# Kernel optimization log

Measured on AMD Instinct MI355X. Metric: run time of the kernel, lower is better.

Reference implementation:

```python
import jax, jax.numpy as jnp
import numpy as np

B, S, D = 4, 2048, 2048
E = 8            # num_experts
TOP_K = 2
H = 1408         # intermediate_size per expert
SH = 2 * H       # shared expert intermediate (shared_experts=2)


def setup_inputs() -> dict:
    key = jax.random.key(0)
    ks = jax.random.split(key, 8)
    sc = 0.02
    return {
        "hidden_states": jax.random.normal(ks[0], (B, S, D), jnp.float32),
        "gate_w": jax.random.normal(ks[1], (E, D), jnp.float32) * sc,   # torch Linear weight [out,in]
        "w1": jax.random.normal(ks[2], (E, H, D), jnp.float32) * sc,    # gate_proj per expert
        "w3": jax.random.normal(ks[3], (E, H, D), jnp.float32) * sc,    # up_proj per expert
        "w2": jax.random.normal(ks[4], (E, D, H), jnp.float32) * sc,    # down_proj per expert
        "sw1": jax.random.normal(ks[5], (SH, D), jnp.float32) * sc,
        "sw3": jax.random.normal(ks[6], (SH, D), jnp.float32) * sc,
        "sw2": jax.random.normal(ks[7], (D, SH), jnp.float32) * sc,
    }


def reference(hidden_states, gate_w, w1, w3, w2, sw1, sw3, sw2):
    b, s, d = hidden_states.shape
    x = hidden_states.reshape(-1, d)                      # [T, D]
    logits = x @ gate_w.T                                 # [T, E]
    rw, sel = jax.lax.top_k(logits, TOP_K)                # [T, K]
    rw = jax.nn.softmax(rw, axis=-1)                      # norm_topk_prob=True
    onehot = jax.nn.one_hot(sel, E, dtype=x.dtype)        # [T, K, E]
    token_mask = onehot.sum(axis=1)                       # [T, E] in {0,1}
    # NOTE: faithful to the source quirk: expert_weights.sum(dim=-1) on a flat
    # masked gather sums routing weights over ALL tokens selecting the expert,
    # producing one scalar per expert.
    s_e = (rw[..., None] * onehot).sum(axis=(0, 1))       # [E]
    combine = token_mask * s_e                            # [T, E]
    # per-expert SwiGLU MLP on all tokens (dense combine form of gather/scatter)
    g = jnp.einsum('td,ehd->eth', x, w1)                  # [E, T, H]
    u = jnp.einsum('td,ehd->eth', x, w3)
    a = jax.nn.silu(g) * u
    y = jnp.einsum('eth,edh->etd', a, w2)                 # [E, T, D]
    out = jnp.einsum('te,etd->td', combine, y)            # [T, D]
    shared = (jax.nn.silu(x @ sw1.T) * (x @ sw3.T)) @ sw2.T
    out = out + shared
    return out.reshape(b, s, d)
```

## Files before the change

kernel.cpp:

```cpp
#include <hip/hip_runtime.h>
#include <hip/hip_bf16.h>
#include <stdint.h>

#define T_TOK 8192
#define DIM   2048
#define NEXP  8
#define HDIM  1408
#define SHDIM 2816

typedef __attribute__((ext_vector_type(8))) short bfrag;
typedef __attribute__((ext_vector_type(4))) float f32x4;

__device__ __forceinline__ short f2bf(float f) {
    union { float f; uint32_t u; } v; v.f = f;
    return (short)((v.u + 0x8000u) >> 16);
}

__device__ __forceinline__ bfrag cvt8(float4 a, float4 b) {
    bfrag r;
    r[0] = f2bf(a.x); r[1] = f2bf(a.y); r[2] = f2bf(a.z); r[3] = f2bf(a.w);
    r[4] = f2bf(b.x); r[5] = f2bf(b.y); r[6] = f2bf(b.z); r[7] = f2bf(b.w);
    return r;
}

__device__ __forceinline__ void gload16(const void* g, void* l) {
    __builtin_amdgcn_global_load_lds(
        (__attribute__((address_space(1))) void*)(g),
        (__attribute__((address_space(3))) void*)(l), 16, 0, 0);
}

#define MFMA16(a, b, c) __builtin_amdgcn_mfma_f32_16x16x32_bf16((a), (b), (c), 0, 0, 0)


__global__ __launch_bounds__(256) void gate_kernel(
    const float* __restrict__ x, const float* __restrict__ gw,
    int* __restrict__ sel, int* __restrict__ meta, float* __restrict__ s_e)
{
    __shared__ float g[NEXP * DIM];
    for (int i = threadIdx.x; i < NEXP * DIM; i += 256) g[i] = gw[i];
    __syncthreads();
    const int wid = threadIdx.x >> 6, lane = threadIdx.x & 63;
    for (int it = 0; it < 8; ++it) {
        const int t = blockIdx.x * 32 + wid * 8 + it;
        float acc[NEXP];
#pragma unroll
        for (int e = 0; e < NEXP; ++e) acc[e] = 0.f;
        const float4* xr = (const float4*)(x + (size_t)t * DIM);
        for (int j = 0; j < DIM / 4; j += 64) {
            float4 xv = xr[j + lane];
#pragma unroll
            for (int e = 0; e < NEXP; ++e) {
                float4 gv = *(const float4*)&g[e * DIM + (j + lane) * 4];
                acc[e] += xv.x * gv.x + xv.y * gv.y + xv.z * gv.z + xv.w * gv.w;
            }
        }
#pragma unroll
        for (int e = 0; e < NEXP; ++e)
            for (int o = 32; o; o >>= 1) acc[e] += __shfl_xor(acc[e], o);
        if (lane == 0) {
            int e0 = 0; float v0 = acc[0];
#pragma unroll
            for (int e = 1; e < NEXP; ++e) if (acc[e] > v0) { v0 = acc[e]; e0 = e; }
            int e1 = -1; float v1 = -3.4e38f;
#pragma unroll
            for (int e = 0; e < NEXP; ++e) if (e != e0 && acc[e] > v1) { v1 = acc[e]; e1 = e; }
            float p0 = 1.f / (1.f + __expf(v1 - v0));
            float p1 = 1.f - p0;
            sel[2 * t] = e0; sel[2 * t + 1] = e1;
            atomicAdd(&s_e[e0], p0); atomicAdd(&s_e[e1], p1);
            atomicAdd(&meta[e0], 1); atomicAdd(&meta[e1], 1);
        }
    }
}

__global__ void scan_kernel(int* meta) {
    if (threadIdx.x == 0) {
        int acc = 0;
        for (int e = 0; e < NEXP; ++e) {
            meta[16 + e] = acc;
            meta[8 + e]  = acc;
            acc += meta[e];
        }
        meta[24] = acc;
    }
}

__global__ __launch_bounds__(256) void fill_kernel(
    const int* __restrict__ sel, int* __restrict__ meta, int* __restrict__ list)
{
    const int t = blockIdx.x * 256 + threadIdx.x;
    int e0 = sel[2 * t], e1 = sel[2 * t + 1];
    int p0 = atomicAdd(&meta[8 + e0], 1); list[p0] = t;
    int p1 = atomicAdd(&meta[8 + e1], 1); list[p1] = t;
}

__global__ __launch_bounds__(256) void cvt_kernel(
    const float* __restrict__ in, __hip_bfloat16* __restrict__ out, int n8)
{
    int i = blockIdx.x * 256 + threadIdx.x;
    const int stride = gridDim.x * 256;
    for (; i < n8; i += stride) {
        const float4* p = (const float4*)(in + (size_t)i * 8);
        float4 a = p[0], b = p[1];
        *(bfrag*)(out + (size_t)i * 8) = cvt8(a, b);
    }
}


template<int N, bool GATHER>
__global__ __launch_bounds__(512, 2) void up_v3(
    const __hip_bfloat16* __restrict__ X,
    const __hip_bfloat16* __restrict__ W1,
    const __hip_bfloat16* __restrict__ W3,
    __hip_bfloat16* __restrict__ act,
    const int* __restrict__ list,
    const int* __restrict__ meta)
{
    constexpr int K = DIM;
    constexpr int NT = K / 64;
    constexpr int nx = N / 128, ny = T_TOK / 256, nz = GATHER ? NEXP : 1;
    constexpr int nwg = nx * ny * nz, cpx = nwg / 8;
    const int bid = (int)blockIdx.x + nx * ((int)blockIdx.y + ny * (int)blockIdx.z);
    const int virt = (bid & 7) * cpx + (bid >> 3);
    const int xi = virt % nx;
    const int rest = virt / nx;
    const int yi = rest % ny;
    const int e = rest / ny;

    int count, base;
    if (GATHER) {
        count = meta[e]; base = meta[16 + e];
        if (yi * 256 >= count) return;
    } else { count = T_TOK; base = 0; }
    const int m0 = yi * 256, n0 = xi * 128;

    __shared__ alignas(16) short As[2][256 * 64];
    __shared__ alignas(16) short B1s[2][128 * 64];
    __shared__ alignas(16) short B3s[2][128 * 64];

    const int tid = threadIdx.x, wid = tid >> 6, lane = tid & 63;
    const int rlo = lane >> 3;
    const int swslot = (lane & 7) ^ rlo;

    const __hip_bfloat16* pA[4];
#pragma unroll
    for (int q = 0; q < 4; ++q) {
        int row = (q * 8 + wid) * 8 + rlo;
        int r = m0 + row; if (r > count - 1) r = count - 1;
        int ga = GATHER ? list[base + r] : r;
        pA[q] = X + (size_t)ga * K + swslot * 8;
    }
    const __hip_bfloat16* pB1[2];
    const __hip_bfloat16* pB3[2];
#pragma unroll
    for (int q = 0; q < 2; ++q) {
        int row = (q * 8 + wid) * 8 + rlo;
        pB1[q] = W1 + ((size_t)e * N + n0 + row) * K + swslot * 8;
        pB3[q] = W3 + ((size_t)e * N + n0 + row) * K + swslot * 8;
    }

#define STAGE_UP(T, BUF) do { const int k0_ = (T) * 64;                         \
    _Pragma("unroll") for (int q = 0; q < 4; ++q)                               \
        gload16(pA[q] + k0_, &As[BUF][(q * 8 + wid) * 512]);                    \
    _Pragma("unroll") for (int q = 0; q < 2; ++q) {                             \
        gload16(pB1[q] + k0_, &B1s[BUF][(q * 8 + wid) * 512]);                  \
        gload16(pB3[q] + k0_, &B3s[BUF][(q * 8 + wid) * 512]); } } while (0)

    const int wm = wid >> 2, wn = wid & 3;
    const int l15 = lane & 15, lhi = lane >> 4;

    f32x4 accg[8][2], accu[8][2];
#pragma unroll
    for (int i = 0; i < 8; ++i)
#pragma unroll
        for (int j = 0; j < 2; ++j) { accg[i][j] = 0.f; accu[i][j] = 0.f; }

    STAGE_UP(0, 0);
    __syncthreads();
    int cur = 0;
#pragma unroll 1
    for (int t = 0; t < NT; ++t) {
        if (t + 1 < NT) STAGE_UP(t + 1, cur ^ 1);
        __builtin_amdgcn_sched_barrier(0);
        bfrag b1f[2][2], b3f[2][2];
#pragma unroll
        for (int j = 0; j < 2; ++j)
#pragma unroll
            for (int kk = 0; kk < 2; ++kk) {
                int rb = wn * 32 + j * 16 + l15;
                int c = kk * 4 + lhi;
                int off = rb * 128 + ((c ^ (rb & 7)) << 4);
                b1f[j][kk] = *(const bfrag*)((const char*)B1s[cur] + off);
                b3f[j][kk] = *(const bfrag*)((const char*)B3s[cur] + off);
            }
        __builtin_amdgcn_s_setprio(1);
#pragma unroll
        for (int i = 0; i < 8; ++i) {
            int ra = wm * 128 + i * 16 + l15;
            const char* abase = (const char*)As[cur] + ra * 128;
            bfrag a0 = *(const bfrag*)(abase + ((lhi       ^ (ra & 7)) << 4));
            bfrag a1 = *(const bfrag*)(abase + (((4 + lhi) ^ (ra & 7)) << 4));
#pragma unroll
            for (int j = 0; j < 2; ++j) {
                accg[i][j] = MFMA16(a0, b1f[j][0], accg[i][j]);
                accu[i][j] = MFMA16(a0, b3f[j][0], accu[i][j]);
                accg[i][j] = MFMA16(a1, b1f[j][1], accg[i][j]);
                accu[i][j] = MFMA16(a1, b3f[j][1], accu[i][j]);
            }
        }
        __builtin_amdgcn_s_setprio(0);
        __syncthreads();
        cur ^= 1;
    }
#undef STAGE_UP

#pragma unroll
    for (int i = 0; i < 8; ++i)
#pragma unroll
        for (int r = 0; r < 4; ++r) {
            int m = wm * 128 + i * 16 + lhi * 4 + r;
            if (m0 + m < count) {
#pragma unroll
                for (int j = 0; j < 2; ++j) {
                    float gg = accg[i][j][r];
                    float uu = accu[i][j][r];
                    float a = gg / (1.f + __expf(-gg)) * uu;
                    int n = n0 + wn * 32 + j * 16 + l15;
                    act[(size_t)(base + m0 + m) * N + n] = __float2bfloat16(a);
                }
            }
        }
}

template<int KD, bool SCATTER>
__global__ __launch_bounds__(512, 2) void down_v3(
    const __hip_bfloat16* __restrict__ A,
    const __hip_bfloat16* __restrict__ W2,
    float* __restrict__ out,
    const int* __restrict__ list,
    const int* __restrict__ meta,
    const float* __restrict__ s_e)
{
    constexpr int N = DIM;
    constexpr int NT = KD / 64;
    constexpr int nx = N / 256, ny = T_TOK / 256, nz = SCATTER ? NEXP : 1;
    constexpr int nwg = nx * ny * nz, cpx = nwg / 8;
    const int bid = (int)blockIdx.x + nx * ((int)blockIdx.y + ny * (int)blockIdx.z);
    const int virt = (bid & 7) * cpx + (bid >> 3);
    const int xi = virt % nx;
    const int rest = virt / nx;
    const int yi = rest % ny;
    const int e = rest / ny;

    int count, base;
    if (SCATTER) {
        count = meta[e]; base = meta[16 + e];
        if (yi * 256 >= count) return;
    } else { count = T_TOK; base = 0; }
    const int m0 = yi * 256, n0 = xi * 256;

    __shared__ alignas(16) short As[2][256 * 64];
    __shared__ alignas(16) short Bs[2][256 * 64];
    __shared__ int tok_s[256];

    const int tid = threadIdx.x, wid = tid >> 6, lane = tid & 63;
    if (SCATTER && tid < 256) {
        int r = m0 + tid; if (r > count - 1) r = count - 1;
        tok_s[tid] = list[base + r];
    }
    const int rlo = lane >> 3;
    const int swslot = (lane & 7) ^ rlo;

    const __hip_bfloat16* pA[4];
    const __hip_bfloat16* pB[4];
#pragma unroll
    for (int q = 0; q < 4; ++q) {
        int row = (q * 8 + wid) * 8 + rlo;
        int r = m0 + row; if (r > count - 1) r = count - 1;
        pA[q] = A  + (size_t)(base + r) * KD + swslot * 8;
        pB[q] = W2 + ((size_t)e * N + n0 + row) * KD + swslot * 8;
    }

#define STAGE_DN(T, BUF) do { const int k0_ = (T) * 64;                         \
    _Pragma("unroll") for (int q = 0; q < 4; ++q) {                             \
        gload16(pA[q] + k0_, &As[BUF][(q * 8 + wid) * 512]);                    \
        gload16(pB[q] + k0_, &Bs[BUF][(q * 8 + wid) * 512]); } } while (0)

    const int wm = wid >> 2, wn = wid & 3;
    const int l15 = lane & 15, lhi = lane >> 4;

    f32x4 acc[8][4];
#pragma unroll
    for (int i = 0; i < 8; ++i)
#pragma unroll
        for (int j = 0; j < 4; ++j) acc[i][j] = 0.f;

    STAGE_DN(0, 0);
    __syncthreads();
    int cur = 0;
#pragma unroll 1
    for (int t = 0; t < NT; ++t) {
        if (t + 1 < NT) STAGE_DN(t + 1, cur ^ 1);
        __builtin_amdgcn_sched_barrier(0);
        bfrag bf[4][2];
#pragma unroll
        for (int j = 0; j < 4; ++j)
#pragma unroll
            for (int kk = 0; kk < 2; ++kk) {
                int rb = wn * 64 + j * 16 + l15;
                int c = kk * 4 + lhi;
                bf[j][kk] = *(const bfrag*)((const char*)Bs[cur] + rb * 128 + ((c ^ (rb & 7)) << 4));
            }
        __builtin_amdgcn_s_setprio(1);
#pragma unroll
        for (int i = 0; i < 8; ++i) {
            int ra = wm * 128 + i * 16 + l15;
            const char* abase = (const char*)As[cur] + ra * 128;
            bfrag a0 = *(const bfrag*)(abase + ((lhi       ^ (ra & 7)) << 4));
            bfrag a1 = *(const bfrag*)(abase + (((4 + lhi) ^ (ra & 7)) << 4));
#pragma unroll
            for (int j = 0; j < 4; ++j) {
                acc[i][j] = MFMA16(a0, bf[j][0], acc[i][j]);
                acc[i][j] = MFMA16(a1, bf[j][1], acc[i][j]);
            }
        }
        __builtin_amdgcn_s_setprio(0);
        __syncthreads();
        cur ^= 1;
    }
#undef STAGE_DN

    const float scale = SCATTER ? s_e[e] : 1.0f;
#pragma unroll
    for (int i = 0; i < 8; ++i)
#pragma unroll
        for (int r = 0; r < 4; ++r) {
            int m = wm * 128 + i * 16 + lhi * 4 + r;
            if (m0 + m < count) {
#pragma unroll
                for (int j = 0; j < 4; ++j) {
                    int n = n0 + wn * 64 + j * 16 + l15;
                    float v = acc[i][j][r] * scale;
                    if (SCATTER) atomicAdd(&out[(size_t)tok_s[m] * DIM + n], v);
                    else         out[(size_t)(m0 + m) * DIM + n] = v;
                }
            }
        }
}

extern "C" void kernel_launch(void* const* d_in, const int* in_sizes, int n_in,
                              void* d_out, int out_size, void* d_ws, size_t ws_size,
                              hipStream_t stream) {
    const float* x   = (const float*)d_in[0];
    const float* gw  = (const float*)d_in[1];
    const float* w1  = (const float*)d_in[2];
    const float* w3  = (const float*)d_in[3];
    const float* w2  = (const float*)d_in[4];
    const float* sw1 = (const float*)d_in[5];
    const float* sw3 = (const float*)d_in[6];
    const float* sw2 = (const float*)d_in[7];
    float* out = (float*)d_out;

    const size_t SZ_X   = (size_t)T_TOK * DIM * 2;
    const size_t SZ_W   = (size_t)NEXP * HDIM * DIM * 2;
    const size_t SZ_SW  = (size_t)SHDIM * DIM * 2;
    const size_t SZ_ACT = (size_t)2 * T_TOK * HDIM * 2;
    const size_t need = SZ_X + 3 * SZ_W + 3 * SZ_SW + SZ_ACT
                      + (size_t)4 * T_TOK * sizeof(int) + 512;
    if (need > ws_size) return;

    char* p = (char*)d_ws;
    __hip_bfloat16* xbf   = (__hip_bfloat16*)p; p += SZ_X;
    __hip_bfloat16* w1bf  = (__hip_bfloat16*)p; p += SZ_W;
    __hip_bfloat16* w3bf  = (__hip_bfloat16*)p; p += SZ_W;
    __hip_bfloat16* w2bf  = (__hip_bfloat16*)p; p += SZ_W;
    __hip_bfloat16* sw1bf = (__hip_bfloat16*)p; p += SZ_SW;
    __hip_bfloat16* sw3bf = (__hip_bfloat16*)p; p += SZ_SW;
    __hip_bfloat16* sw2bf = (__hip_bfloat16*)p; p += SZ_SW;
    __hip_bfloat16* act   = (__hip_bfloat16*)p; p += SZ_ACT;
    int* list = (int*)p; p += (size_t)2 * T_TOK * sizeof(int);
    int* sel  = (int*)p; p += (size_t)2 * T_TOK * sizeof(int);
    int* meta = (int*)p;
    float* s_e = (float*)(meta + 32);

    hipMemsetAsync(meta, 0, 256, stream);
    gate_kernel<<<T_TOK / 32, 256, 0, stream>>>(x, gw, sel, meta, s_e);
    scan_kernel<<<1, 64, 0, stream>>>(meta);
    fill_kernel<<<T_TOK / 256, 256, 0, stream>>>(sel, meta, list);

    cvt_kernel<<<2048, 256, 0, stream>>>(x,   xbf,   T_TOK * DIM / 8);
    cvt_kernel<<<2048, 256, 0, stream>>>(w1,  w1bf,  NEXP * HDIM * DIM / 8);
    cvt_kernel<<<2048, 256, 0, stream>>>(w3,  w3bf,  NEXP * HDIM * DIM / 8);
    cvt_kernel<<<2048, 256, 0, stream>>>(w2,  w2bf,  NEXP * HDIM * DIM / 8);
    cvt_kernel<<<2048, 256, 0, stream>>>(sw1, sw1bf, SHDIM * DIM / 8);
    cvt_kernel<<<2048, 256, 0, stream>>>(sw3, sw3bf, SHDIM * DIM / 8);
    cvt_kernel<<<2048, 256, 0, stream>>>(sw2, sw2bf, SHDIM * DIM / 8);

    up_v3<SHDIM, false><<<dim3(SHDIM / 128, T_TOK / 256, 1), 512, 0, stream>>>(
        xbf, sw1bf, sw3bf, act, nullptr, meta);
    down_v3<SHDIM, false><<<dim3(DIM / 256, T_TOK / 256, 1), 512, 0, stream>>>(
        act, sw2bf, out, nullptr, meta, s_e);
    up_v3<HDIM, true><<<dim3(HDIM / 128, T_TOK / 256, NEXP), 512, 0, stream>>>(
        xbf, w1bf, w3bf, act, list, meta);
    down_v3<HDIM, true><<<dim3(DIM / 256, T_TOK / 256, NEXP), 512, 0, stream>>>(
        act, w2bf, out, list, meta, s_e);
}
```

Measured before the change: 1.181 ms.

## Split K-tiles into half stages, fuse conversions, replace atomic scatter with combine pass

The GEMM main loops now split each 64-wide K tile into two 32-wide sub-stages. Each sub-stage is prefetched one step ahead and guarded by explicit vmcnt waits and barriers instead of full __syncthreads, with a new 4-slot LDS swizzle. The x-to-bf16 conversion moves into the gate kernel, and the six weight conversions are fused into one launch. The routed down-projection writes bf16 per-slot outputs to a scratch buffer that aliases the start of the workspace, and a new combine kernel adds the weighted results per token, replacing float atomics. This aims to remove atomic contention, launch overhead and pipeline stalls. It adds bf16 rounding of expert outputs and a workspace aliasing risk, since yscr overlaps xbf and the converted weights.

```diff
diff --git a/kernel.cpp b/kernel.cpp
--- a/kernel.cpp
+++ b/kernel.cpp
@@ -10,10 +10,15 @@
 
 typedef __attribute__((ext_vector_type(8))) short bfrag;
 typedef __attribute__((ext_vector_type(4))) float f32x4;
+typedef __attribute__((ext_vector_type(4))) short s16x4;
 
 __device__ __forceinline__ short f2bf(float f) {
     union { float f; uint32_t u; } v; v.f = f;
     return (short)((v.u + 0x8000u) >> 16);
+}
+__device__ __forceinline__ float bf2f(short s) {
+    union { uint32_t u; float f; } v; v.u = ((uint32_t)(uint16_t)s) << 16;
+    return v.f;
 }
 
 __device__ __forceinline__ bfrag cvt8(float4 a, float4 b) {
@@ -30,10 +35,12 @@
 }
 
 #define MFMA16(a, b, c) __builtin_amdgcn_mfma_f32_16x16x32_bf16((a), (b), (c), 0, 0, 0)
+#define SWZ4(r) (((r) & 3) ^ (((r) >> 2) & 3))
 
 
 __global__ __launch_bounds__(256) void gate_kernel(
     const float* __restrict__ x, const float* __restrict__ gw,
+    __hip_bfloat16* __restrict__ xbf,
     int* __restrict__ sel, int* __restrict__ meta, float* __restrict__ s_e)
 {
     __shared__ float g[NEXP * DIM];
@@ -48,6 +55,8 @@
         const float4* xr = (const float4*)(x + (size_t)t * DIM);
         for (int j = 0; j < DIM / 4; j += 64) {
             float4 xv = xr[j + lane];
+            s16x4 xv16 = { f2bf(xv.x), f2bf(xv.y), f2bf(xv.z), f2bf(xv.w) };
+            *(s16x4*)&xbf[(size_t)t * DIM + (j + lane) * 4] = xv16;
 #pragma unroll
             for (int e = 0; e < NEXP; ++e) {
                 float4 gv = *(const float4*)&g[e * DIM + (j + lane) * 4];
@@ -86,29 +95,46 @@
 }
 
 __global__ __launch_bounds__(256) void fill_kernel(
-    const int* __restrict__ sel, int* __restrict__ meta, int* __restrict__ list)
+    const int* __restrict__ sel, int* __restrict__ meta,
+    int* __restrict__ list, int2* __restrict__ slots)
 {
     const int t = blockIdx.x * 256 + threadIdx.x;
     int e0 = sel[2 * t], e1 = sel[2 * t + 1];
     int p0 = atomicAdd(&meta[8 + e0], 1); list[p0] = t;
     int p1 = atomicAdd(&meta[8 + e1], 1); list[p1] = t;
-}
-
-__global__ __launch_bounds__(256) void cvt_kernel(
-    const float* __restrict__ in, __hip_bfloat16* __restrict__ out, int n8)
-{
-    int i = blockIdx.x * 256 + threadIdx.x;
+    slots[t] = make_int2(p0, p1);
+}
+
+#define C1 2883584
+#define C2 5767168
+#define C3 8650752
+#define C4 9371648
+#define C5 10092544
+#define C6 10813440
+__global__ __launch_bounds__(256) void cvt6_kernel(
+    const float* __restrict__ s0, const float* __restrict__ s1, const float* __restrict__ s2,
+    const float* __restrict__ s3, const float* __restrict__ s4, const float* __restrict__ s5,
+    __hip_bfloat16* __restrict__ d0, __hip_bfloat16* __restrict__ d1, __hip_bfloat16* __restrict__ d2,
+    __hip_bfloat16* __restrict__ d3, __hip_bfloat16* __restrict__ d4, __hip_bfloat16* __restrict__ d5)
+{
     const int stride = gridDim.x * 256;
-    for (; i < n8; i += stride) {
-        const float4* p = (const float4*)(in + (size_t)i * 8);
+    for (int i = blockIdx.x * 256 + threadIdx.x; i < C6; i += stride) {
+        const float* s; __hip_bfloat16* d; int off;
+        if      (i < C1) { s = s0; d = d0; off = i; }
+        else if (i < C2) { s = s1; d = d1; off = i - C1; }
+        else if (i < C3) { s = s2; d = d2; off = i - C2; }
+        else if (i < C4) { s = s3; d = d3; off = i - C3; }
+        else if (i < C5) { s = s4; d = d4; off = i - C4; }
+        else             { s = s5; d = d5; off = i - C5; }
+        const float4* p = (const float4*)(s + (size_t)off * 8);
         float4 a = p[0], b = p[1];
-        *(bfrag*)(out + (size_t)i * 8) = cvt8(a, b);
+        *(bfrag*)(d + (size_t)off * 8) = cvt8(a, b);
     }
 }
 
 
 template<int N, bool GATHER>
-__global__ __launch_bounds__(512, 2) void up_v3(
+__global__ __launch_bounds__(512, 2) void up_v4(
     const __hip_bfloat16* __restrict__ X,
     const __hip_bfloat16* __restrict__ W1,
     const __hip_bfloat16* __restrict__ W3,
@@ -134,40 +160,33 @@
     } else { count = T_TOK; base = 0; }
     const int m0 = yi * 256, n0 = xi * 128;
 
-    __shared__ alignas(16) short As[2][256 * 64];
-    __shared__ alignas(16) short B1s[2][128 * 64];
-    __shared__ alignas(16) short B3s[2][128 * 64];
+    __shared__ alignas(16) short As[2][2][256 * 32];
+    __shared__ alignas(16) short B1s[2][2][128 * 32];
+    __shared__ alignas(16) short B3s[2][2][128 * 32];
 
     const int tid = threadIdx.x, wid = tid >> 6, lane = tid & 63;
-    const int rlo = lane >> 3;
-    const int swslot = (lane & 7) ^ rlo;
-
-    const __hip_bfloat16* pA[4];
-#pragma unroll
-    for (int q = 0; q < 4; ++q) {
-        int row = (q * 8 + wid) * 8 + rlo;
-        int r = m0 + row; if (r > count - 1) r = count - 1;
+    const int srow = tid >> 2, dslot = tid & 3;
+    const int sswz = dslot ^ SWZ4(srow);
+
+    const __hip_bfloat16* pA[2];
+#pragma unroll
+    for (int q = 0; q < 2; ++q) {
+        int r = m0 + q * 128 + srow; if (r > count - 1) r = count - 1;
         int ga = GATHER ? list[base + r] : r;
-        pA[q] = X + (size_t)ga * K + swslot * 8;
-    }
-    const __hip_bfloat16* pB1[2];
-    const __hip_bfloat16* pB3[2];
-#pragma unroll
-    for (int q = 0; q < 2; ++q) {
-        int row = (q * 8 + wid) * 8 + rlo;
-        pB1[q] = W1 + ((size_t)e * N + n0 + row) * K + swslot * 8;
-        pB3[q] = W3 + ((size_t)e * N + n0 + row) * K + swslot * 8;
-    }
-
-#define STAGE_UP(T, BUF) do { const int k0_ = (T) * 64;                         \
-    _Pragma("unroll") for (int q = 0; q < 4; ++q)                               \
-        gload16(pA[q] + k0_, &As[BUF][(q * 8 + wid) * 512]);                    \
-    _Pragma("unroll") for (int q = 0; q < 2; ++q) {                             \
-        gload16(pB1[q] + k0_, &B1s[BUF][(q * 8 + wid) * 512]);                  \
-        gload16(pB3[q] + k0_, &B3s[BUF][(q * 8 + wid) * 512]); } } while (0)
+        pA[q] = X + (size_t)ga * K + sswz * 8;
+    }
+    const __hip_bfloat16* pB1 = W1 + ((size_t)e * N + n0 + srow) * K + sswz * 8;
+    const __hip_bfloat16* pB3 = W3 + ((size_t)e * N + n0 + srow) * K + sswz * 8;
+
+#define STAGE_UP(K0, KK, BUF) do {                                              \
+    gload16(pA[0] + (K0) + (KK) * 32, &As[BUF][KK][tid * 8]);                   \
+    gload16(pA[1] + (K0) + (KK) * 32, &As[BUF][KK][4096 + tid * 8]);            \
+    gload16(pB1   + (K0) + (KK) * 32, &B1s[BUF][KK][tid * 8]);                  \
+    gload16(pB3   + (K0) + (KK) * 32, &B3s[BUF][KK][tid * 8]); } while (0)
 
     const int wm = wid >> 2, wn = wid & 3;
     const int l15 = lane & 15, lhi = lane >> 4;
+    const int lswz = (lhi ^ SWZ4(l15)) * 8;
 
     f32x4 accg[8][2], accu[8][2];
 #pragma unroll
@@ -175,44 +194,46 @@
 #pragma unroll
         for (int j = 0; j < 2; ++j) { accg[i][j] = 0.f; accu[i][j] = 0.f; }
 
-    STAGE_UP(0, 0);
-    __syncthreads();
-    int cur = 0;
+    STAGE_UP(0, 0, 0);
+    STAGE_UP(0, 1, 0);
+    asm volatile("s_waitcnt vmcnt(4)" ::: "memory");
+    __builtin_amdgcn_s_barrier();
+    __builtin_amdgcn_sched_barrier(0);
+
 #pragma unroll 1
     for (int t = 0; t < NT; ++t) {
-        if (t + 1 < NT) STAGE_UP(t + 1, cur ^ 1);
-        __builtin_amdgcn_sched_barrier(0);
-        bfrag b1f[2][2], b3f[2][2];
-#pragma unroll
-        for (int j = 0; j < 2; ++j)
-#pragma unroll
-            for (int kk = 0; kk < 2; ++kk) {
+        const int cur = t & 1;
+        const int tpk0 = (t + 1 < NT ? t + 1 : NT - 1) * 64;
+#pragma unroll
+        for (int kk = 0; kk < 2; ++kk) {
+            bfrag b1f[2], b3f[2];
+#pragma unroll
+            for (int j = 0; j < 2; ++j) {
                 int rb = wn * 32 + j * 16 + l15;
-                int c = kk * 4 + lhi;
-                int off = rb * 128 + ((c ^ (rb & 7)) << 4);
-                b1f[j][kk] = *(const bfrag*)((const char*)B1s[cur] + off);
-                b3f[j][kk] = *(const bfrag*)((const char*)B3s[cur] + off);
-            }
-        __builtin_amdgcn_s_setprio(1);
-#pragma unroll
-        for (int i = 0; i < 8; ++i) {
-            int ra = wm * 128 + i * 16 + l15;
-            const char* abase = (const char*)As[cur] + ra * 128;
-            bfrag a0 = *(const bfrag*)(abase + ((lhi       ^ (ra & 7)) << 4));
-            bfrag a1 = *(const bfrag*)(abase + (((4 + lhi) ^ (ra & 7)) << 4));
-#pragma unroll
-            for (int j = 0; j < 2; ++j) {
-                accg[i][j] = MFMA16(a0, b1f[j][0], accg[i][j]);
-                accu[i][j] = MFMA16(a0, b3f[j][0], accu[i][j]);
-                accg[i][j] = MFMA16(a1, b1f[j][1], accg[i][j]);
-                accu[i][j] = MFMA16(a1, b3f[j][1], accu[i][j]);
-            }
-        }
-        __builtin_amdgcn_s_setprio(0);
-        __syncthreads();
-        cur ^= 1;
+                b1f[j] = *(const bfrag*)&B1s[cur][kk][rb * 32 + lswz];
+                b3f[j] = *(const bfrag*)&B3s[cur][kk][rb * 32 + lswz];
+            }
+            STAGE_UP(tpk0, kk, cur ^ 1);
+            __builtin_amdgcn_s_barrier();
+            __builtin_amdgcn_s_setprio(1);
+#pragma unroll
+            for (int i = 0; i < 8; ++i) {
+                int ra = wm * 128 + i * 16 + l15;
+                bfrag a = *(const bfrag*)&As[cur][kk][ra * 32 + lswz];
+#pragma unroll
+                for (int j = 0; j < 2; ++j) {
+                    accg[i][j] = MFMA16(a, b1f[j], accg[i][j]);
+                    accu[i][j] = MFMA16(a, b3f[j], accu[i][j]);
+                }
+            }
+            __builtin_amdgcn_s_setprio(0);
+            asm volatile("s_waitcnt vmcnt(4)" ::: "memory");
+            __builtin_amdgcn_s_barrier();
+            __builtin_amdgcn_sched_barrier(0);
+        }
     }
 #undef STAGE_UP
+    asm volatile("s_waitcnt vmcnt(0)" ::: "memory");
 
 #pragma unroll
     for (int i = 0; i < 8; ++i)
@@ -232,18 +253,17 @@
         }
 }
 
-template<int KD, bool SCATTER>
-__global__ __launch_bounds__(512, 2) void down_v3(
+template<int KD, bool TO_BF16>
+__global__ __launch_bounds__(512, 2) void down_v4(
     const __hip_bfloat16* __restrict__ A,
     const __hip_bfloat16* __restrict__ W2,
     float* __restrict__ out,
-    const int* __restrict__ list,
-    const int* __restrict__ meta,
-    const float* __restrict__ s_e)
+    __hip_bfloat16* __restrict__ yscr,
+    const int* __restrict__ meta)
 {
     constexpr int N = DIM;
     constexpr int NT = KD / 64;
-    constexpr int nx = N / 256, ny = T_TOK / 256, nz = SCATTER ? NEXP : 1;
+    constexpr int nx = N / 256, ny = T_TOK / 256, nz = TO_BF16 ? NEXP : 1;
     constexpr int nwg = nx * ny * nz, cpx = nwg / 8;
     const int bid = (int)blockIdx.x + nx * ((int)blockIdx.y + ny * (int)blockIdx.z);
     const int virt = (bid & 7) * cpx + (bid >> 3);
@@ -253,41 +273,37 @@
     const int e = rest / ny;
 
     int count, base;
-    if (SCATTER) {
+    if (TO_BF16) {
         count = meta[e]; base = meta[16 + e];
         if (yi * 256 >= count) return;
     } else { count = T_TOK; base = 0; }
     const int m0 = yi * 256, n0 = xi * 256;
 
-    __shared__ alignas(16) short As[2][256 * 64];
-    __shared__ alignas(16) short Bs[2][256 * 64];
-    __shared__ int tok_s[256];
+    __shared__ alignas(16) short As[2][2][256 * 32];
+    __shared__ alignas(16) short Bs[2][2][256 * 32];
 
     const int tid = threadIdx.x, wid = tid >> 6, lane = tid & 63;
-    if (SCATTER && tid < 256) {
-        int r = m0 + tid; if (r > count - 1) r = count - 1;
-        tok_s[tid] = list[base + r];
-    }
-    const int rlo = lane >> 3;
-    const int swslot = (lane & 7) ^ rlo;
-
-    const __hip_bfloat16* pA[4];
-    const __hip_bfloat16* pB[4];
-#pragma unroll
-    for (int q = 0; q < 4; ++q) {
-        int row = (q * 8 + wid) * 8 + rlo;
-        int r = m0 + row; if (r > count - 1) r = count - 1;
-        pA[q] = A  + (size_t)(base + r) * KD + swslot * 8;
-        pB[q] = W2 + ((size_t)e * N + n0 + row) * KD + swslot * 8;
-    }
-
-#define STAGE_DN(T, BUF) do { const int k0_ = (T) * 64;                         \
-    _Pragma("unroll") for (int q = 0; q < 4; ++q) {                             \
-        gload16(pA[q] + k0_, &As[BUF][(q * 8 + wid) * 512]);                    \
-        gload16(pB[q] + k0_, &Bs[BUF][(q * 8 + wid) * 512]); } } while (0)
+    const int srow = tid >> 2, dslot = tid & 3;
+    const int sswz = dslot ^ SWZ4(srow);
+
+    const __hip_bfloat16* pA[2];
+    const __hip_bfloat16* pB[2];
+#pragma unroll
+    for (int q = 0; q < 2; ++q) {
+        int r = m0 + q * 128 + srow; if (r > count - 1) r = count - 1;
+        pA[q] = A  + (size_t)(base + r) * KD + sswz * 8;
+        pB[q] = W2 + ((size_t)e * N + n0 + q * 128 + srow) * KD + sswz * 8;
+    }
+
+#define STAGE_DN(K0, KK, BUF) do {                                              \
+    gload16(pA[0] + (K0) + (KK) * 32, &As[BUF][KK][tid * 8]);                   \
+    gload16(pA[1] + (K0) + (KK) * 32, &As[BUF][KK][4096 + tid * 8]);            \
+    gload16(pB[0] + (K0) + (KK) * 32, &Bs[BUF][KK][tid * 8]);                   \
+    gload16(pB[1] + (K0) + (KK) * 32, &Bs[BUF][KK][4096 + tid * 8]); } while (0)
 
     const int wm = wid >> 2, wn = wid & 3;
     const int l15 = lane & 15, lhi = lane >> 4;
+    const int lswz = (lhi ^ SWZ4(l15)) * 8;
 
     f32x4 acc[8][4];
 #pragma unroll
@@ -295,42 +311,44 @@
 #pragma unroll
         for (int j = 0; j < 4; ++j) acc[i][j] = 0.f;
 
-    STAGE_DN(0, 0);
-    __syncthreads();
-    int cur = 0;
+    STAGE_DN(0, 0, 0);
+    STAGE_DN(0, 1, 0);
+    asm volatile("s_waitcnt vmcnt(4)" ::: "memory");
+    __builtin_amdgcn_s_barrier();
+    __builtin_amdgcn_sched_barrier(0);
+
 #pragma unroll 1
     for (int t = 0; t < NT; ++t) {
-        if (t + 1 < NT) STAGE_DN(t + 1, cur ^ 1);
-        __builtin_amdgcn_sched_barrier(0);
-        bfrag bf[4][2];
-#pragma unroll
-        for (int j = 0; j < 4; ++j)
-#pragma unroll
-            for (int kk = 0; kk < 2; ++kk) {
+        const int cur = t & 1;
+        const int tpk0 = (t + 1 < NT ? t + 1 : NT - 1) * 64;
+#pragma unroll
+        for (int kk = 0; kk < 2; ++kk) {
+            bfrag bf[4];
+#pragma unroll
+            for (int j = 0; j < 4; ++j) {
                 int rb = wn * 64 + j * 16 + l15;
-                int c = kk * 4 + lhi;
-                bf[j][kk] = *(const bfrag*)((const char*)Bs[cur] + rb * 128 + ((c ^ (rb & 7)) << 4));
-            }
-        __builtin_amdgcn_s_setprio(1);
-#pragma unroll
-        for (int i = 0; i < 8; ++i) {
-            int ra = wm * 128 + i * 16 + l15;
-            const char* abase = (const char*)As[cur] + ra * 128;
-            bfrag a0 = *(const bfrag*)(abase + ((lhi       ^ (ra & 7)) << 4));
-            bfrag a1 = *(const bfrag*)(abase + (((4 + lhi) ^ (ra & 7)) << 4));
-#pragma unroll
-            for (int j = 0; j < 4; ++j) {
-                acc[i][j] = MFMA16(a0, bf[j][0], acc[i][j]);
-                acc[i][j] = MFMA16(a1, bf[j][1], acc[i][j]);
-            }
-        }
-        __builtin_amdgcn_s_setprio(0);
-        __syncthreads();
-        cur ^= 1;
+                bf[j] = *(const bfrag*)&Bs[cur][kk][rb * 32 + lswz];
+            }
+            STAGE_DN(tpk0, kk, cur ^ 1);
+            __builtin_amdgcn_s_barrier();
+            __builtin_amdgcn_s_setprio(1);
+#pragma unroll
+            for (int i = 0; i < 8; ++i) {
+                int ra = wm * 128 + i * 16 + l15;
+                bfrag a = *(const bfrag*)&As[cur][kk][ra * 32 + lswz];
+#pragma unroll
+                for (int j = 0; j < 4; ++j)
+                    acc[i][j] = MFMA16(a, bf[j], acc[i][j]);
+            }
+            __builtin_amdgcn_s_setprio(0);
+            asm volatile("s_waitcnt vmcnt(4)" ::: "memory");
+            __builtin_amdgcn_s_barrier();
+            __builtin_amdgcn_sched_barrier(0);
+        }
     }
 #undef STAGE_DN
-
-    const float scale = SCATTER ? s_e[e] : 1.0f;
+    asm volatile("s_waitcnt vmcnt(0)" ::: "memory");
+
 #pragma unroll
     for (int i = 0; i < 8; ++i)
 #pragma unroll
@@ -340,12 +358,38 @@
 #pragma unroll
                 for (int j = 0; j < 4; ++j) {
                     int n = n0 + wn * 64 + j * 16 + l15;
-                    float v = acc[i][j][r] * scale;
-                    if (SCATTER) atomicAdd(&out[(size_t)tok_s[m] * DIM + n], v);
-                    else         out[(size_t)(m0 + m) * DIM + n] = v;
+                    if (TO_BF16)
+                        yscr[(size_t)(base + m0 + m) * DIM + n] = __float2bfloat16(acc[i][j][r]);
+                    else
+                        out[(size_t)(m0 + m) * DIM + n] = acc[i][j][r];
                 }
             }
         }
+}
+
+__global__ __launch_bounds__(256) void combine_kernel(
+    float* __restrict__ out, const __hip_bfloat16* __restrict__ yscr,
+    const int* __restrict__ sel, const int2* __restrict__ slots,
+    const float* __restrict__ s_e)
+{
+    const int t = blockIdx.x;
+    const int d = threadIdx.x * 8;
+    const int2 sl = slots[t];
+    const float se0 = s_e[sel[2 * t]];
+    const float se1 = s_e[sel[2 * t + 1]];
+    bfrag y0 = *(const bfrag*)&yscr[(size_t)sl.x * DIM + d];
+    bfrag y1 = *(const bfrag*)&yscr[(size_t)sl.y * DIM + d];
+    float4* o = (float4*)(out + (size_t)t * DIM + d);
+    float4 o0 = o[0], o1 = o[1];
+    o0.x += se0 * bf2f(y0[0]) + se1 * bf2f(y1[0]);
+    o0.y += se0 * bf2f(y0[1]) + se1 * bf2f(y1[1]);
+    o0.z += se0 * bf2f(y0[2]) + se1 * bf2f(y1[2]);
+    o0.w += se0 * bf2f(y0[3]) + se1 * bf2f(y1[3]);
+    o1.x += se0 * bf2f(y0[4]) + se1 * bf2f(y1[4]);
+    o1.y += se0 * bf2f(y0[5]) + se1 * bf2f(y1[5]);
+    o1.z += se0 * bf2f(y0[6]) + se1 * bf2f(y1[6]);
+    o1.w += se0 * bf2f(y0[7]) + se1 * bf2f(y1[7]);
+    o[0] = o0; o[1] = o1;
 }
 
 extern "C" void kernel_launch(void* const* d_in, const int* in_sizes, int n_in,
@@ -366,7 +410,8 @@
     const size_t SZ_SW  = (size_t)SHDIM * DIM * 2;
     const size_t SZ_ACT = (size_t)2 * T_TOK * HDIM * 2;
     const size_t need = SZ_X + 3 * SZ_W + 3 * SZ_SW + SZ_ACT
-                      + (size_t)4 * T_TOK * sizeof(int) + 512;
+                      + (size_t)4 * T_TOK * sizeof(int)
+                      + (size_t)2 * T_TOK * sizeof(int)  + 512;
     if (need > ws_size) return;
 
     char* p = (char*)d_ws;
@@ -378,30 +423,28 @@
     __hip_bfloat16* sw3bf = (__hip_bfloat16*)p; p += SZ_SW;
     __hip_bfloat16* sw2bf = (__hip_bfloat16*)p; p += SZ_SW;
     __hip_bfloat16* act   = (__hip_bfloat16*)p; p += SZ_ACT;
-    int* list = (int*)p; p += (size_t)2 * T_TOK * sizeof(int);
-    int* sel  = (int*)p; p += (size_t)2 * T_TOK * sizeof(int);
-    int* meta = (int*)p;
-    float* s_e = (float*)(meta + 32);
+    int*  list  = (int*)p;  p += (size_t)2 * T_TOK * sizeof(int);
+    int*  sel   = (int*)p;  p += (size_t)2 * T_TOK * sizeof(int);
+    int2* slots = (int2*)p; p += (size_t)2 * T_TOK * sizeof(int);
+    int*  meta  = (int*)p;
+    float* s_e  = (float*)(meta + 32);
+    __hip_bfloat16* yscr = (__hip_bfloat16*)d_ws;
 
     hipMemsetAsync(meta, 0, 256, stream);
-    gate_kernel<<<T_TOK / 32, 256, 0, stream>>>(x, gw, sel, meta, s_e);
+    gate_kernel<<<T_TOK / 32, 256, 0, stream>>>(x, gw, xbf, sel, meta, s_e);
     scan_kernel<<<1, 64, 0, stream>>>(meta);
-    fill_kernel<<<T_TOK / 256, 256, 0, stream>>>(sel, meta, list);
-
-    cvt_kernel<<<2048, 256, 0, stream>>>(x,   xbf,   T_TOK * DIM / 8);
-    cvt_kernel<<<2048, 256, 0, stream>>>(w1,  w1bf,  NEXP * HDIM * DIM / 8);
-    cvt_kernel<<<2048, 256, 0, stream>>>(w3,  w3bf,  NEXP * HDIM * DIM / 8);
-    cvt_kernel<<<2048, 256, 0, stream>>>(w2,  w2bf,  NEXP * HDIM * DIM / 8);
-    cvt_kernel<<<2048, 256, 0, stream>>>(sw1, sw1bf, SHDIM * DIM / 8);
-    cvt_kernel<<<2048, 256, 0, stream>>>(sw3, sw3bf, SHDIM * DIM / 8);
-    cvt_kernel<<<2048, 256, 0, stream>>>(sw2, sw2bf, SHDIM * DIM / 8);
-
-    up_v3<SHDIM, false><<<dim3(SHDIM / 128, T_TOK / 256, 1), 512, 0, stream>>>(
+    fill_kernel<<<T_TOK / 256, 256, 0, stream>>>(sel, meta, list, slots);
+
+    cvt6_kernel<<<2048, 256, 0, stream>>>(w1, w3, w2, sw1, sw3, sw2,
+                                          w1bf, w3bf, w2bf, sw1bf, sw3bf, sw2bf);
+
+    up_v4<SHDIM, false><<<dim3(SHDIM / 128, T_TOK / 256, 1), 512, 0, stream>>>(
         xbf, sw1bf, sw3bf, act, nullptr, meta);
-    down_v3<SHDIM, false><<<dim3(DIM / 256, T_TOK / 256, 1), 512, 0, stream>>>(
-        act, sw2bf, out, nullptr, meta, s_e);
-    up_v3<HDIM, true><<<dim3(HDIM / 128, T_TOK / 256, NEXP), 512, 0, stream>>>(
+    down_v4<SHDIM, false><<<dim3(DIM / 256, T_TOK / 256, 1), 512, 0, stream>>>(
+        act, sw2bf, out, nullptr, meta);
+    up_v4<HDIM, true><<<dim3(HDIM / 128, T_TOK / 256, NEXP), 512, 0, stream>>>(
         xbf, w1bf, w3bf, act, list, meta);
-    down_v3<HDIM, true><<<dim3(DIM / 256, T_TOK / 256, NEXP), 512, 0, stream>>>(
-        act, w2bf, out, list, meta, s_e);
-}
+    down_v4<HDIM, true><<<dim3(DIM / 256, T_TOK / 256, NEXP), 512, 0, stream>>>(
+        act, w2bf, out, yscr, meta);
+    combine_kernel<<<T_TOK, 256, 0, stream>>>(out, yscr, sel, slots, s_e);
+}
```

Measured after the change: 1.267 ms. 7.3% more time.
